# Kernel optimization log

Hardware: AMD Instinct MI355X
Metric: run time of the kernel (lower is better)

Reference implementation:

```python
import jax, jax.numpy as jnp
import numpy as np

# Representative Blocks2Matrix configuration: single coupled block key
# (l1=2, l2=2, lambda=2), one atom type with 8 radial channels.
N_SYS = 16        # number of systems
N_ATOMS = 64      # atoms per system
L1, L2, LAM = 2, 2, 2
NRAD = 8          # radial channels per (l, Z)
S = 32768         # number of atom-pair samples across all systems
M1, M2, MU = 2 * L1 + 1, 2 * L2 + 1, 2 * LAM + 1
NORB_ATOM = NRAD * M1            # orbitals per atom (radial-major, mu-minor; see make_orbital_map)
N = N_ATOMS * NORB_ATOM          # 2560 orbitals per system


def setup_inputs() -> dict:
    key = jax.random.key(0)
    k1, k2, k3, k4, k5 = jax.random.split(key, 5)
    values = jax.random.normal(k1, (S, MU, NRAD * NRAD), dtype=jnp.float32)
    cg = jax.random.normal(k2, (M1, M2, MU), dtype=jnp.float32)
    sys_idx = jax.random.randint(k3, (S,), 0, N_SYS)
    i_idx = jax.random.randint(k4, (S,), 0, N_ATOMS)
    j_idx = jax.random.randint(k5, (S,), 0, N_ATOMS)
    return {"values": values, "cg": cg, "sys_idx": sys_idx,
            "i_idx": i_idx, "j_idx": j_idx}


def reference(values, cg, sys_idx, i_idx, j_idx):
    # Decouple: uncoupled[s, m1, m2, n1, n2] = sum_mu cg[m1, m2, mu] * values[s, mu, n1, n2]
    vals = values.reshape(S, MU, NRAD, NRAD)
    # orbital ordering is radial-major, mu-minor -> index (n, m)
    blocks = jnp.einsum('abm,smpq->spaqb', cg, vals)  # [S, n1, m1, n2, m2]
    blocks = blocks.reshape(S, NORB_ATOM, NORB_ATOM)
    # Global orbital indices for each pair's block rows/cols
    ar = jnp.arange(NORB_ATOM)
    rows = i_idx[:, None] * NORB_ATOM + ar  # [S, 40]
    cols = j_idx[:, None] * NORB_ATOM + ar  # [S, 40]
    H = jnp.zeros((N_SYS, N, N), dtype=values.dtype)
    # Scatter block at (i, j) and its transpose at (j, i) (Hermitian build)
    H = H.at[sys_idx[:, None, None], rows[:, :, None], cols[:, None, :]].add(blocks)
    H = H.at[sys_idx[:, None, None], cols[:, :, None], rows[:, None, :]].add(
        jnp.swapaxes(blocks, 1, 2))
    return H
```

## Files before the change

kernel.cpp:

```cpp
#include <hip/hip_runtime.h>


#define SS      32768
#define MU      5
#define NORB    40
#define NSYS    16
#define NATOMS  64
#define NDIM    2560
#define NBINS   (NSYS * NATOMS * NATOMS)
#define CAP     16
#define MAXOVF  8192

#define WS_NEEDED   (524288 + (size_t)NBINS * CAP * 4)

__global__ __launch_bounds__(256) void b2m_fill(
    const int* __restrict__ sys_idx, const int* __restrict__ i_idx,
    const int* __restrict__ j_idx,
    int* __restrict__ counts, int* __restrict__ bins,
    int* __restrict__ ovf_cnt, int2* __restrict__ ovf)
{
    int s = blockIdx.x * blockDim.x + threadIdx.x;
    if (s >= SS) return;
    int sy = sys_idx[s], i = i_idx[s], j = j_idx[s];

    int bd = (sy * NATOMS + i) * NATOMS + j;
    int pos = atomicAdd(&counts[bd], 1);
    if (pos < CAP) bins[bd * CAP + pos] = s;
    else { int o = atomicAdd(ovf_cnt, 1); if (o < MAXOVF) ovf[o] = make_int2(bd, s); }

    int bt = (sy * NATOMS + j) * NATOMS + i;
    int st = s | 0x10000;
    pos = atomicAdd(&counts[bt], 1);
    if (pos < CAP) bins[bt * CAP + pos] = st;
    else { int o = atomicAdd(ovf_cnt, 1); if (o < MAXOVF) ovf[o] = make_int2(bt, st); }
}

__global__ __launch_bounds__(320) void b2m_gather(
    const float* __restrict__ values, const float* __restrict__ cg,
    const int* __restrict__ counts, const int* __restrict__ bins,
    float* __restrict__ H)
{
    __shared__ float sv[MU * 64];
    __shared__ float scg[125];

    const int bin = blockIdx.x;
    const int tid = threadIdx.x;
    if (tid < 125) scg[tid] = cg[tid];

    const int j  = bin & 63;
    const int i  = (bin >> 6) & 63;
    const int sy = bin >> 12;

    int r_[5], c_[5];
    #pragma unroll
    for (int it = 0; it < 5; ++it) {
        int e = tid + it * 320;
        r_[it] = e / 40;
        c_[it] = e - r_[it] * 40;
    }

    float acc[5] = {0.f, 0.f, 0.f, 0.f, 0.f};
    int n = counts[bin];
    if (n > CAP) n = CAP;
    __syncthreads();

    for (int k = 0; k < n; ++k) {
        int  ent = bins[bin * CAP + k];
        int  s   = ent & 0xFFFF;
        bool tr  = (ent >> 16) != 0;
        sv[tid] = values[(size_t)s * (MU * 64) + tid];
        __syncthreads();
        #pragma unroll
        for (int it = 0; it < 5; ++it) {
            int R = tr ? c_[it] : r_[it];
            int C = tr ? r_[it] : c_[it];
            int p = R / 5, a = R - p * 5;
            int q = C / 5, b = C - q * 5;
            #pragma unroll
            for (int m = 0; m < 5; ++m)
                acc[it] = fmaf(scg[(a * 5 + b) * 5 + m], sv[m * 64 + p * 8 + q], acc[it]);
        }
        __syncthreads();
    }

    float* Hs = H + (size_t)sy * NDIM * NDIM;
    const int rowbase = i * NORB, colbase = j * NORB;
    #pragma unroll
    for (int it = 0; it < 5; ++it)
        Hs[(size_t)(rowbase + r_[it]) * NDIM + (colbase + c_[it])] = acc[it];
}

__global__ __launch_bounds__(256) void b2m_ovf_apply(
    const float* __restrict__ values, const float* __restrict__ cg,
    const int* __restrict__ ovf_cnt, const int2* __restrict__ ovf,
    float* __restrict__ H)
{
    int n = *ovf_cnt;
    if (n > MAXOVF) n = MAXOVF;
    for (int k = blockIdx.x; k < n; k += gridDim.x) {
        int  bin = ovf[k].x;
        int  ent = ovf[k].y;
        int  s   = ent & 0xFFFF;
        bool tr  = (ent >> 16) != 0;
        int  j = bin & 63, i = (bin >> 6) & 63, sy = bin >> 12;
        const float* vs = values + (size_t)s * (MU * 64);
        float* Hs = H + (size_t)sy * NDIM * NDIM;
        for (int e = threadIdx.x; e < 1600; e += blockDim.x) {
            int rr = e / 40, cc = e - rr * 40;
            int R = tr ? cc : rr, C = tr ? rr : cc;
            int p = R / 5, a = R - p * 5;
            int q = C / 5, b = C - q * 5;
            float v = 0.f;
            for (int m = 0; m < 5; ++m)
                v = fmaf(cg[(a * 5 + b) * 5 + m], vs[m * 64 + p * 8 + q], v);
            atomicAdd(Hs + (size_t)(i * NORB + rr) * NDIM + (j * NORB + cc), v);
        }
    }
}

__global__ __launch_bounds__(320) void b2m_scatter(
    const float* __restrict__ values, const float* __restrict__ cg,
    const int* __restrict__ sys_idx, const int* __restrict__ i_idx,
    const int* __restrict__ j_idx, float* __restrict__ H)
{
    __shared__ float sv[MU * 64];
    __shared__ float scg[125];
    const int s = blockIdx.x, tid = threadIdx.x;
    if (tid < MU * 64) sv[tid] = values[(size_t)s * (MU * 64) + tid];
    if (tid < 125) scg[tid] = cg[tid];
    __syncthreads();
    const int sys = sys_idx[s], i = i_idx[s], j = j_idx[s];
    float* Hs = H + (size_t)sys * NDIM * NDIM;
    const int rowbase = i * NORB, colbase = j * NORB;
    #pragma unroll
    for (int it = 0; it < 5; ++it) {
        const int e = tid + it * 320;
        const int r = e / 40, c = e - r * 40;
        const int p = r / 5, a = r - p * 5, q = c / 5, b = c - q * 5;
        float v = 0.f;
        #pragma unroll
        for (int m = 0; m < 5; ++m)
            v = fmaf(scg[(a * 5 + b) * 5 + m], sv[m * 64 + p * 8 + q], v);
        atomicAdd(Hs + (size_t)(rowbase + r) * NDIM + (colbase + c), v);
    }
    #pragma unroll
    for (int it = 0; it < 5; ++it) {
        const int e = tid + it * 320;
        const int c2 = e / 40, r2 = e - c2 * 40;
        const int p = r2 / 5, a = r2 - p * 5, q = c2 / 5, b = c2 - q * 5;
        float v = 0.f;
        #pragma unroll
        for (int m = 0; m < 5; ++m)
            v = fmaf(scg[(a * 5 + b) * 5 + m], sv[m * 64 + p * 8 + q], v);
        atomicAdd(Hs + (size_t)(colbase + c2) * NDIM + (rowbase + r2), v);
    }
}

extern "C" void kernel_launch(void* const* d_in, const int* in_sizes, int n_in,
                              void* d_out, int out_size, void* d_ws, size_t ws_size,
                              hipStream_t stream) {
    const float* values  = (const float*)d_in[0];
    const float* cg      = (const float*)d_in[1];
    const int*   sys_idx = (const int*)d_in[2];
    const int*   i_idx   = (const int*)d_in[3];
    const int*   j_idx   = (const int*)d_in[4];
    float*       H       = (float*)d_out;

    if (ws_size >= WS_NEEDED) {
        char* ws      = (char*)d_ws;
        int*  counts  = (int*)ws;
        int*  ovf_cnt = (int*)(ws + 262144);
        int2* ovf     = (int2*)(ws + 262272);
        int*  bins    = (int*)(ws + 524288);

        hipMemsetAsync(ws, 0, 262400, stream);

        b2m_fill<<<(SS + 255) / 256, 256, 0, stream>>>(
            sys_idx, i_idx, j_idx, counts, bins, ovf_cnt, ovf);
        b2m_gather<<<NBINS, 320, 0, stream>>>(values, cg, counts, bins, H);
        b2m_ovf_apply<<<64, 256, 0, stream>>>(values, cg, ovf_cnt, ovf, H);
    } else {
        hipMemsetAsync(H, 0, (size_t)out_size * sizeof(float), stream);
        b2m_scatter<<<SS, 320, 0, stream>>>(values, cg, sys_idx, i_idx, j_idx, H);
    }
}
```

Before: 625.2 us.

## Sum values per bin before decoupling and process bins per wavefront

The gather kernel now assigns each 64-lane wavefront a contiguous range of bins. Because the decoupling is linear, each lane first sums the values of all direct entries and all transposed entries in the bin, then applies the CG contraction once per bin instead of once per entry. This removes the per-entry block syncs and repeated FMAs. Output rows go through a per-wave LDS staging buffer so the writes to H coalesce. In exchange each lane keeps 25 accumulators, and one wave handles many bins serially, so load balance and occupancy change.

```diff
diff --git a/kernel.cpp b/kernel.cpp
--- a/kernel.cpp
+++ b/kernel.cpp
@@ -2,7 +2,6 @@
 
 
 #define SS      32768
-#define MU      5
 #define NORB    40
 #define NSYS    16
 #define NATOMS  64
@@ -10,6 +9,10 @@
 #define NBINS   (NSYS * NATOMS * NATOMS)
 #define CAP     16
 #define MAXOVF  8192
+#define GBLK    2048
+#define TPB     256
+#define WPB     (TPB / 64)
+#define BPW     (NBINS / (GBLK * WPB))
 
 #define WS_NEEDED   (524288 + (size_t)NBINS * CAP * 4)
 
@@ -35,59 +38,103 @@
     else { int o = atomicAdd(ovf_cnt, 1); if (o < MAXOVF) ovf[o] = make_int2(bt, st); }
 }
 
-__global__ __launch_bounds__(320) void b2m_gather(
+#define ENTRY_BODY(ENT) do {                                            \
+    int _ent = (ENT);                                                   \
+    const float* _vb = values + (size_t)(_ent & 0xFFFF) * 320;          \
+    if ((_ent & 0x10000) == 0) {                                        \
+        ++nD;                                                           \
+        _Pragma("unroll")                                               \
+        for (int m = 0; m < 5; ++m) vsD[m] += _vb[m * 64 + lane];       \
+    } else {                                                            \
+        ++nT;                                                           \
+        _Pragma("unroll")                                               \
+        for (int m = 0; m < 5; ++m) vsT[m] += _vb[m * 64 + bsl];        \
+    }                                                                   \
+} while (0)
+
+__global__ __launch_bounds__(TPB) void b2m_gather(
     const float* __restrict__ values, const float* __restrict__ cg,
     const int* __restrict__ counts, const int* __restrict__ bins,
     float* __restrict__ H)
 {
-    __shared__ float sv[MU * 64];
-    __shared__ float scg[125];
-
-    const int bin = blockIdx.x;
-    const int tid = threadIdx.x;
+    __shared__ float scg[128];
+    __shared__ float stage[WPB][320];
+
+    const int tid  = threadIdx.x;
+    const int lane = tid & 63;
+    const int w    = tid >> 6;
+
     if (tid < 125) scg[tid] = cg[tid];
-
-    const int j  = bin & 63;
-    const int i  = (bin >> 6) & 63;
-    const int sy = bin >> 12;
-
-    int r_[5], c_[5];
+    __syncthreads();
+
+    const int p   = lane >> 3, q = lane & 7;
+    const int bsl = (q << 3) | p;
+
+    int soff[5];
     #pragma unroll
     for (int it = 0; it < 5; ++it) {
-        int e = tid + it * 320;
-        r_[it] = e / 40;
-        c_[it] = e - r_[it] * 40;
-    }
-
-    float acc[5] = {0.f, 0.f, 0.f, 0.f, 0.f};
-    int n = counts[bin];
-    if (n > CAP) n = CAP;
-    __syncthreads();
-
-    for (int k = 0; k < n; ++k) {
-        int  ent = bins[bin * CAP + k];
-        int  s   = ent & 0xFFFF;
-        bool tr  = (ent >> 16) != 0;
-        sv[tid] = values[(size_t)s * (MU * 64) + tid];
-        __syncthreads();
-        #pragma unroll
-        for (int it = 0; it < 5; ++it) {
-            int R = tr ? c_[it] : r_[it];
-            int C = tr ? r_[it] : c_[it];
-            int p = R / 5, a = R - p * 5;
-            int q = C / 5, b = C - q * 5;
-            #pragma unroll
-            for (int m = 0; m < 5; ++m)
-                acc[it] = fmaf(scg[(a * 5 + b) * 5 + m], sv[m * 64 + p * 8 + q], acc[it]);
-        }
-        __syncthreads();
-    }
-
-    float* Hs = H + (size_t)sy * NDIM * NDIM;
-    const int rowbase = i * NORB, colbase = j * NORB;
-    #pragma unroll
-    for (int it = 0; it < 5; ++it)
-        Hs[(size_t)(rowbase + r_[it]) * NDIM + (colbase + c_[it])] = acc[it];
+        int e = it * 64 + lane;
+        int srow = e / 40, scol = e - srow * 40;
+        soff[it] = srow * 5 * NDIM + scol;
+    }
+
+    const int gw = __builtin_amdgcn_readfirstlane((int)blockIdx.x * WPB + w);
+    const int t0 = gw * BPW;
+    float* const sw = stage[w];
+
+    for (int t = t0; t < t0 + BPW; ++t) {
+        int n = counts[t];
+        if (n > CAP) n = CAP;
+
+        float vsD[5] = {0.f, 0.f, 0.f, 0.f, 0.f};
+        float vsT[5] = {0.f, 0.f, 0.f, 0.f, 0.f};
+        int nD = 0, nT = 0;
+
+        if (n > 0) {
+            int4 e4 = *reinterpret_cast<const int4*>(bins + (size_t)t * CAP);
+            ENTRY_BODY(e4.x);
+            if (n > 1) ENTRY_BODY(e4.y);
+            if (n > 2) ENTRY_BODY(e4.z);
+            if (n > 3) ENTRY_BODY(e4.w);
+            for (int k = 4; k < n; ++k)
+                ENTRY_BODY(bins[(size_t)t * CAP + k]);
+        }
+
+        float acc[25];
+        #pragma unroll
+        for (int i2 = 0; i2 < 25; ++i2) acc[i2] = 0.f;
+
+        if (nD) {
+            #pragma unroll
+            for (int a = 0; a < 5; ++a)
+                #pragma unroll
+                for (int b = 0; b < 5; ++b)
+                    #pragma unroll
+                    for (int m = 0; m < 5; ++m)
+                        acc[a * 5 + b] = fmaf(scg[(a * 5 + b) * 5 + m], vsD[m], acc[a * 5 + b]);
+        }
+        if (nT) {
+            #pragma unroll
+            for (int a = 0; a < 5; ++a)
+                #pragma unroll
+                for (int b = 0; b < 5; ++b)
+                    #pragma unroll
+                    for (int m = 0; m < 5; ++m)
+                        acc[a * 5 + b] = fmaf(scg[(b * 5 + a) * 5 + m], vsT[m], acc[a * 5 + b]);
+        }
+
+        const int jj = t & 63, ii = (t >> 6) & 63, sy = t >> 12;
+        float* Hs = H + ((size_t)sy * NDIM + (size_t)ii * NORB) * NDIM + (size_t)jj * NORB;
+        #pragma unroll
+        for (int g = 0; g < 5; ++g) {
+            #pragma unroll
+            for (int b = 0; b < 5; ++b)
+                sw[p * 40 + q * 5 + b] = acc[g * 5 + b];
+            #pragma unroll
+            for (int it = 0; it < 5; ++it)
+                Hs[(size_t)(soff[it] + g * NDIM)] = sw[it * 64 + lane];
+        }
+    }
 }
 
 __global__ __launch_bounds__(256) void b2m_ovf_apply(
@@ -103,16 +150,16 @@
         int  s   = ent & 0xFFFF;
         bool tr  = (ent >> 16) != 0;
         int  j = bin & 63, i = (bin >> 6) & 63, sy = bin >> 12;
-        const float* vs = values + (size_t)s * (MU * 64);
+        const float* vs = values + (size_t)s * 320;
         float* Hs = H + (size_t)sy * NDIM * NDIM;
         for (int e = threadIdx.x; e < 1600; e += blockDim.x) {
             int rr = e / 40, cc = e - rr * 40;
             int R = tr ? cc : rr, C = tr ? rr : cc;
-            int p = R / 5, a = R - p * 5;
-            int q = C / 5, b = C - q * 5;
+            int pp = R / 5, a = R - pp * 5;
+            int qq = C / 5, b = C - qq * 5;
             float v = 0.f;
             for (int m = 0; m < 5; ++m)
-                v = fmaf(cg[(a * 5 + b) * 5 + m], vs[m * 64 + p * 8 + q], v);
+                v = fmaf(cg[(a * 5 + b) * 5 + m], vs[m * 64 + pp * 8 + qq], v);
             atomicAdd(Hs + (size_t)(i * NORB + rr) * NDIM + (j * NORB + cc), v);
         }
     }
@@ -123,10 +170,10 @@
     const int* __restrict__ sys_idx, const int* __restrict__ i_idx,
     const int* __restrict__ j_idx, float* __restrict__ H)
 {
-    __shared__ float sv[MU * 64];
+    __shared__ float svv[320];
     __shared__ float scg[125];
     const int s = blockIdx.x, tid = threadIdx.x;
-    if (tid < MU * 64) sv[tid] = values[(size_t)s * (MU * 64) + tid];
+    if (tid < 320) svv[tid] = values[(size_t)s * 320 + tid];
     if (tid < 125) scg[tid] = cg[tid];
     __syncthreads();
     const int sys = sys_idx[s], i = i_idx[s], j = j_idx[s];
@@ -136,22 +183,22 @@
     for (int it = 0; it < 5; ++it) {
         const int e = tid + it * 320;
         const int r = e / 40, c = e - r * 40;
-        const int p = r / 5, a = r - p * 5, q = c / 5, b = c - q * 5;
+        const int pp = r / 5, a = r - pp * 5, qq = c / 5, b = c - qq * 5;
         float v = 0.f;
         #pragma unroll
         for (int m = 0; m < 5; ++m)
-            v = fmaf(scg[(a * 5 + b) * 5 + m], sv[m * 64 + p * 8 + q], v);
+            v = fmaf(scg[(a * 5 + b) * 5 + m], svv[m * 64 + pp * 8 + qq], v);
         atomicAdd(Hs + (size_t)(rowbase + r) * NDIM + (colbase + c), v);
     }
     #pragma unroll
     for (int it = 0; it < 5; ++it) {
         const int e = tid + it * 320;
         const int c2 = e / 40, r2 = e - c2 * 40;
-        const int p = r2 / 5, a = r2 - p * 5, q = c2 / 5, b = c2 - q * 5;
+        const int pp = r2 / 5, a = r2 - pp * 5, qq = c2 / 5, b = c2 - qq * 5;
         float v = 0.f;
         #pragma unroll
         for (int m = 0; m < 5; ++m)
-            v = fmaf(scg[(a * 5 + b) * 5 + m], sv[m * 64 + p * 8 + q], v);
+            v = fmaf(scg[(a * 5 + b) * 5 + m], svv[m * 64 + pp * 8 + qq], v);
         atomicAdd(Hs + (size_t)(colbase + c2) * NDIM + (rowbase + r2), v);
     }
 }
@@ -177,7 +224,7 @@
 
         b2m_fill<<<(SS + 255) / 256, 256, 0, stream>>>(
             sys_idx, i_idx, j_idx, counts, bins, ovf_cnt, ovf);
-        b2m_gather<<<NBINS, 320, 0, stream>>>(values, cg, counts, bins, H);
+        b2m_gather<<<GBLK, TPB, 0, stream>>>(values, cg, counts, bins, H);
         b2m_ovf_apply<<<64, 256, 0, stream>>>(values, cg, ovf_cnt, ovf, H);
     } else {
         hipMemsetAsync(H, 0, (size_t)out_size * sizeof(float), stream);
```

Result: no change. 617.4 us (-1.3%).
